# Performance work log

Measured on AMD Instinct MI355X. Metric: run time of the kernel, lower is better.

The kernel has to match this reference:

```python
import jax, jax.numpy as jnp
import numpy as np

E = 1024   # embed_dim
H = 16     # num_heads
R = 256    # rank
HD = E // H
B, S = 2, 2048


def setup_inputs() -> dict:
    key = jax.random.key(0)
    ks = jax.random.split(key, 20)
    sc = 0.02
    d = {
        'query': jax.random.normal(ks[0], (B, S, E), jnp.float32),
        'key':   jax.random.normal(ks[1], (B, S, E), jnp.float32),
        'value': jax.random.normal(ks[2], (B, S, E), jnp.float32),
    }
    names = ['q', 'k', 'v', 'o']
    i = 3
    for n in names:
        d[f'W{n}_lo'] = jax.random.normal(ks[i], (E, R), jnp.float32) * sc; i += 1
        d[f'b{n}_lo'] = jnp.zeros((R,), jnp.float32)
        d[f'W{n}_hi'] = jax.random.normal(ks[i], (R, E), jnp.float32) * sc; i += 1
        d[f'b{n}_hi'] = jnp.zeros((E,), jnp.float32)
    return d


def _lowrank(x, W_lo, b_lo, W_hi, b_hi):
    # Linear(E->R) then Linear(R->E)
    return (x @ W_lo + b_lo) @ W_hi + b_hi


def reference(query, key, value,
              Wq_lo, bq_lo, Wq_hi, bq_hi,
              Wk_lo, bk_lo, Wk_hi, bk_hi,
              Wv_lo, bv_lo, Wv_hi, bv_hi,
              Wo_lo, bo_lo, Wo_hi, bo_hi):
    b, s, _ = query.shape
    q = _lowrank(query, Wq_lo, bq_lo, Wq_hi, bq_hi)
    k = _lowrank(key,   Wk_lo, bk_lo, Wk_hi, bk_hi)
    v = _lowrank(value, Wv_lo, bv_lo, Wv_hi, bv_hi)
    # (B, S, E) -> (B, H, S, HD)
    q = q.reshape(b, s, H, HD).transpose(0, 2, 1, 3)
    k = k.reshape(b, s, H, HD).transpose(0, 2, 1, 3)
    v = v.reshape(b, s, H, HD).transpose(0, 2, 1, 3)
    scores = jnp.einsum('bhqd,bhkd->bhqk', q, k) / jnp.sqrt(jnp.float32(HD))
    attn = jax.nn.softmax(scores, axis=-1)  # dropout p=0.0 -> identity
    out = jnp.einsum('bhqk,bhkd->bhqd', attn, v)
    out = out.transpose(0, 2, 1, 3).reshape(b, s, E)
    return _lowrank(out, Wo_lo, bo_lo, Wo_hi, bo_hi)
```

## Files before the change

### kernel.cpp

```cpp
#include <hip/hip_runtime.h>

namespace {

constexpr int kE  = 1024;
constexpr int kH  = 16;
constexpr int kR  = 256;
constexpr int kHD = 64;
constexpr int kB  = 2;
constexpr int kS  = 2048;
constexpr int kM  = kB * kS;

typedef float  floatx4 __attribute__((ext_vector_type(4)));
typedef short  short8  __attribute__((ext_vector_type(8)));
typedef short  short4  __attribute__((ext_vector_type(4)));
typedef unsigned int uint2v __attribute__((ext_vector_type(2)));

__device__ inline short f2bf(float f) {
  union { float f; unsigned u; } x{f};
  unsigned r = x.u + 0x7FFF + ((x.u >> 16) & 1);
  return (short)(r >> 16);
}

__device__ inline unsigned cvt_pk_bf16(float a, float b) {
#if defined(__HIP_DEVICE_COMPILE__)
  unsigned r;
  asm("v_cvt_pk_bf16_f32 %0, %1, %2" : "=v"(r) : "v"(a), "v"(b));
  return r;
#else
  return (unsigned)(unsigned short)f2bf(a) | ((unsigned)(unsigned short)f2bf(b) << 16);
#endif
}

__device__ inline short4 pack2(unsigned a, unsigned b) {
  union { uint2v u; short4 s; } x;
  x.u[0] = a; x.u[1] = b;
  return x.s;
}

__device__ inline float fexp2(float x) {
#if defined(__HIP_DEVICE_COMPILE__) && __has_builtin(__builtin_amdgcn_exp2f)
  return __builtin_amdgcn_exp2f(x);
#else
  return exp2f(x);
#endif
}

__device__ inline void async_copy16(const void* g, void* l) {
  __builtin_amdgcn_global_load_lds(
      (const __attribute__((address_space(1))) unsigned int*)g,
      (__attribute__((address_space(3))) unsigned int*)l,
      16, 0, 0);
}

#if defined(__HIP_DEVICE_COMPILE__)
  #if __has_builtin(__builtin_amdgcn_mfma_f32_16x16x16bf16_1k)
    #define MFMA16(a, b, c) __builtin_amdgcn_mfma_f32_16x16x16bf16_1k(a, b, c, 0, 0, 0)
  #elif __has_builtin(__builtin_amdgcn_mfma_f32_16x16x16_bf16)
    #define MFMA16(a, b, c) __builtin_amdgcn_mfma_f32_16x16x16_bf16(a, b, c, 0, 0, 0)
  #else
    #error "no 16x16x16 bf16 MFMA builtin on device"
  #endif
#else
  #define MFMA16(a, b, c) (c)
#endif

struct PrepArgs { const float* src[8]; short* dst[8]; };

__global__ __launch_bounds__(256) void prep_weights(PrepArgs pa) {
  const int id = blockIdx.y;
  const bool lo = (id & 1) == 0;
  const int K = lo ? 1024 : 256;
  const int N = lo ? 256 : 1024;
  const int tiles_k = K >> 6;
  const int k0 = (blockIdx.x % tiles_k) * 64;
  const int n0 = (blockIdx.x / tiles_k) * 64;
  const float* src = pa.src[id];
  short* dst = pa.dst[id];

  __shared__ float tile[64][68];
  const int t  = threadIdx.x;
  const int c4 = (t & 15) * 4;
  const int r  = t >> 4;

#pragma unroll
  for (int i = 0; i < 4; ++i) {
    const int rk = r + i * 16;
    *(float4*)&tile[rk][c4] = *(const float4*)&src[(size_t)(k0 + rk) * N + n0 + c4];
  }
  __syncthreads();
#pragma unroll
  for (int i = 0; i < 4; ++i) {
    const int rn = r + i * 16;
    short4 o = { f2bf(tile[c4 + 0][rn]), f2bf(tile[c4 + 1][rn]),
                 f2bf(tile[c4 + 2][rn]), f2bf(tile[c4 + 3][rn]) };
    *(short4*)&dst[(size_t)(n0 + rn) * K + k0 + c4] = o;
  }
}

__global__ __launch_bounds__(256) void convert_in(
    const float* q, const float* k, const float* v,
    short* xq, short* xk, short* xv)
{
  const float* srcs[3] = {q, k, v};
  short* dsts[3] = {xq, xk, xv};
  const float* s = srcs[blockIdx.y];
  short* d = dsts[blockIdx.y];
  const size_t i = ((size_t)blockIdx.x * 256 + threadIdx.x) * 8;
  float4 a = *(const float4*)(s + i);
  float4 b = *(const float4*)(s + i + 4);
  short8 o = { f2bf(a.x), f2bf(a.y), f2bf(a.z), f2bf(a.w),
               f2bf(b.x), f2bf(b.y), f2bf(b.z), f2bf(b.w) };
  *(short8*)(d + i) = o;
}

struct GemmArgs {
  const short* A[3]; const short* Bt[3]; const float* bias[3];
  void* C[3]; float scale[3];
};

template <int N, int K, int BM, int BN, int MODE>
__global__ __launch_bounds__(256) void gemm_bf16(GemmArgs args) {
  constexpr int TILES_N = N / BN;
  constexpr int WTM = BM / 2, WTN = BN / 2;
  constexpr int FI = WTM / 16, FJ = WTN / 16;
  constexpr int AROUNDS = (BM * 64) / 4096;
  constexpr int BROUNDS = (BN * 64) / 4096;

  const int z = blockIdx.y;
  const int row0 = (blockIdx.x / TILES_N) * BM;
  const int col0 = (blockIdx.x % TILES_N) * BN;
  const short* A  = args.A[z];
  const short* Bt = args.Bt[z];
  const float* bias = args.bias[z];
  const float scale = args.scale[z];

  __shared__ short As[BM * 32];
  __shared__ short Bs[BN * 32];

  const int t    = threadIdx.x;
  const int wave = t >> 6;
  const int lane = t & 63;
  const int lq   = lane & 15;
  const int quad = lane >> 4;
  const int wm0  = (wave >> 1) * WTM;
  const int wn0  = (wave & 1) * WTN;

  const int srow = t >> 2;
  const int scol = (t & 3) * 8;

  floatx4 acc[FI][FJ] = {};

  for (int kk = 0; kk < K; kk += 32) {
#pragma unroll
    for (int r = 0; r < AROUNDS; ++r)
      async_copy16(A + (size_t)(row0 + r * 64 + srow) * K + kk + scol,
                   (char*)As + r * 4096 + wave * 1024);
#pragma unroll
    for (int r = 0; r < BROUNDS; ++r)
      async_copy16(Bt + (size_t)(col0 + r * 64 + srow) * K + kk + scol,
                   (char*)Bs + r * 4096 + wave * 1024);
    __syncthreads();

    short8 af[FI], bf[FJ];
#pragma unroll
    for (int i = 0; i < FI; ++i)
      af[i] = *(const short8*)((const char*)As + ((wm0 + i * 16 + lq) * 64 + quad * 16));
#pragma unroll
    for (int j = 0; j < FJ; ++j)
      bf[j] = *(const short8*)((const char*)Bs + ((wn0 + j * 16 + lq) * 64 + quad * 16));
#pragma unroll
    for (int i = 0; i < FI; ++i)
#pragma unroll
      for (int j = 0; j < FJ; ++j)
        acc[i][j] = __builtin_amdgcn_mfma_f32_16x16x32_bf16(af[i], bf[j], acc[i][j], 0, 0, 0);
    __syncthreads();
  }

#pragma unroll
  for (int i = 0; i < FI; ++i) {
    const int rbase = row0 + wm0 + i * 16 + quad * 4;
#pragma unroll
    for (int j = 0; j < FJ; ++j) {
      const int col = col0 + wn0 + j * 16 + lq;
      const float bj = bias[col];
      if (MODE == 2) {
        float* C = (float*)args.C[z];
#pragma unroll
        for (int r = 0; r < 4; ++r)
          C[(size_t)(rbase + r) * N + col] = (acc[i][j][r] + bj) * scale;
      } else if (MODE == 1) {
        short* C = (short*)args.C[z];
        const int h = col >> 6, d = col & 63;
        const int b = rbase >> 11, s = rbase & 2047;
        if (z == 2) {
          short4 o = { f2bf(acc[i][j][0] + bj), f2bf(acc[i][j][1] + bj),
                       f2bf(acc[i][j][2] + bj), f2bf(acc[i][j][3] + bj) };
          *(short4*)&C[((size_t)((b * 16 + h) * 64 + d)) * 2048 + s] = o;
        } else {
#pragma unroll
          for (int r = 0; r < 4; ++r)
            C[((size_t)((b * 16 + h) * 2048 + s + r)) * 64 + d] =
                f2bf((acc[i][j][r] + bj) * scale);
        }
      } else {
        short* C = (short*)args.C[z];
#pragma unroll
        for (int r = 0; r < 4; ++r)
          C[(size_t)(rbase + r) * N + col] = f2bf((acc[i][j][r] + bj) * scale);
      }
    }
  }
}

__global__ __launch_bounds__(256) void attn_mfma(
    const short* __restrict__ Qp, const short* __restrict__ Kp,
    const short* __restrict__ Vtp, short* __restrict__ O)
{
  __shared__ short Ks[64][72];
  __shared__ short Vs[64][72];

  const int t    = threadIdx.x;
  const int wave = t >> 6;
  const int lane = t & 63;
  const int lq   = lane & 15;
  const int quad = lane >> 4;

  const int q0 = blockIdx.x * 128;
  const int bh = blockIdx.y;
  const int b  = bh >> 4;
  const int h  = bh & 15;

  short8 qf0[2], qf1[2];
#pragma unroll
  for (int qt = 0; qt < 2; ++qt) {
    const short* qrow = Qp + ((size_t)bh * kS + q0 + wave * 32 + qt * 16 + lq) * 64;
    qf0[qt] = *(const short8*)(qrow + quad * 8);
    qf1[qt] = *(const short8*)(qrow + 32 + quad * 8);
  }

  const short* Kbase = Kp  + (size_t)bh * kS * 64;
  const short* Vbase = Vtp + (size_t)bh * 64 * kS;

  const int srow = wave * 16 + (lane >> 3);
  const int scol = (lane & 7) * 8;

  floatx4 Oacc[4][2] = {};
  float m[2] = {-1e30f, -1e30f};
  float l[2] = {0.f, 0.f};

  short8 gk0 = *(const short8*)(Kbase + (size_t)(srow) * 64 + scol);
  short8 gk1 = *(const short8*)(Kbase + (size_t)(srow + 8) * 64 + scol);
  short8 gv0 = *(const short8*)(Vbase + (size_t)srow * kS + scol);
  short8 gv1 = *(const short8*)(Vbase + (size_t)(srow + 8) * kS + scol);

  for (int kc = 0; kc < kS; kc += 64) {
    __syncthreads();
    *(short8*)&Ks[srow][scol]     = gk0;
    *(short8*)&Ks[srow + 8][scol] = gk1;
    *(short8*)&Vs[srow][scol]     = gv0;
    *(short8*)&Vs[srow + 8][scol] = gv1;
    __syncthreads();

    if (kc + 64 < kS) {
      gk0 = *(const short8*)(Kbase + (size_t)(kc + 64 + srow) * 64 + scol);
      gk1 = *(const short8*)(Kbase + (size_t)(kc + 64 + srow + 8) * 64 + scol);
      gv0 = *(const short8*)(Vbase + (size_t)srow * kS + kc + 64 + scol);
      gv1 = *(const short8*)(Vbase + (size_t)(srow + 8) * kS + kc + 64 + scol);
    }

    floatx4 Sc[4][2];
#pragma unroll
    for (int tt = 0; tt < 4; ++tt) {
      short8 a0 = *(const short8*)&Ks[tt * 16 + lq][quad * 8];
      short8 a1 = *(const short8*)&Ks[tt * 16 + lq][32 + quad * 8];
#pragma unroll
      for (int qt = 0; qt < 2; ++qt) {
        floatx4 c = {};
        c = __builtin_amdgcn_mfma_f32_16x16x32_bf16(a0, qf0[qt], c, 0, 0, 0);
        c = __builtin_amdgcn_mfma_f32_16x16x32_bf16(a1, qf1[qt], c, 0, 0, 0);
        Sc[tt][qt] = c;
      }
    }

    short4 pf[4][2];
#pragma unroll
    for (int qt = 0; qt < 2; ++qt) {
      float x0 = fmaxf(fmaxf(Sc[0][qt][0], Sc[0][qt][1]), fmaxf(Sc[0][qt][2], Sc[0][qt][3]));
      float x1 = fmaxf(fmaxf(Sc[1][qt][0], Sc[1][qt][1]), fmaxf(Sc[1][qt][2], Sc[1][qt][3]));
      float x2 = fmaxf(fmaxf(Sc[2][qt][0], Sc[2][qt][1]), fmaxf(Sc[2][qt][2], Sc[2][qt][3]));
      float x3 = fmaxf(fmaxf(Sc[3][qt][0], Sc[3][qt][1]), fmaxf(Sc[3][qt][2], Sc[3][qt][3]));
      float plane = fmaxf(fmaxf(x0, x1), fmaxf(x2, x3));

      if (!__all(plane <= m[qt] + 10.f)) {
        float mc = fmaxf(plane, __shfl_xor(plane, 16, 64));
        mc = fmaxf(mc, __shfl_xor(mc, 32, 64));
        const float mn = fmaxf(m[qt], mc);
        const float a = fexp2(m[qt] - mn);
        m[qt] = mn;
        l[qt] *= a;
#pragma unroll
        for (int dt = 0; dt < 4; ++dt) Oacc[dt][qt] *= a;
      }

      float ls = 0.f;
#pragma unroll
      for (int tt = 0; tt < 4; ++tt) {
        float p0 = fexp2(Sc[tt][qt][0] - m[qt]);
        float p1 = fexp2(Sc[tt][qt][1] - m[qt]);
        float p2 = fexp2(Sc[tt][qt][2] - m[qt]);
        float p3 = fexp2(Sc[tt][qt][3] - m[qt]);
        ls += (p0 + p1) + (p2 + p3);
        pf[tt][qt] = pack2(cvt_pk_bf16(p0, p1), cvt_pk_bf16(p2, p3));
      }
      l[qt] += ls;
    }

#pragma unroll
    for (int dt = 0; dt < 4; ++dt) {
#pragma unroll
      for (int tt = 0; tt < 4; ++tt) {
        short4 vf = *(const short4*)&Vs[dt * 16 + lq][tt * 16 + quad * 4];
#pragma unroll
        for (int qt = 0; qt < 2; ++qt)
          Oacc[dt][qt] = MFMA16(vf, pf[tt][qt], Oacc[dt][qt]);
      }
    }
  }

#pragma unroll
  for (int qt = 0; qt < 2; ++qt) {
    float lv = l[qt];
    lv += __shfl_xor(lv, 16, 64);
    lv += __shfl_xor(lv, 32, 64);
    const float inv = 1.f / lv;

    short* orow = O + ((size_t)(b * kS + q0 + wave * 32 + qt * 16 + lq)) * kE + h * kHD;
#pragma unroll
    for (int dt = 0; dt < 4; ++dt) {
      short4 o = pack2(cvt_pk_bf16(Oacc[dt][qt][0] * inv, Oacc[dt][qt][1] * inv),
                       cvt_pk_bf16(Oacc[dt][qt][2] * inv, Oacc[dt][qt][3] * inv));
      *(short4*)&orow[dt * 16 + quad * 4] = o;
    }
  }
}

}

extern "C" void kernel_launch(void* const* d_in, const int* in_sizes, int n_in,
                              void* d_out, int out_size, void* d_ws, size_t ws_size,
                              hipStream_t stream) {
  short* ws = (short*)d_ws;
  short* Xq  = ws;
  short* Xk  = Xq  + (size_t)kM * kE;
  short* Xv  = Xk  + (size_t)kM * kE;
  short* Tq  = Xv  + (size_t)kM * kE;
  short* Tk  = Tq  + (size_t)kM * kR;
  short* Tv  = Tk  + (size_t)kM * kR;
  short* Qh  = Tv  + (size_t)kM * kR;
  short* Kh  = Qh  + (size_t)kM * kE;
  short* Vth = Kh  + (size_t)kM * kE;
  short* Ab  = Vth + (size_t)kM * kE;
  short* To  = Ab  + (size_t)kM * kE;
  short* Wt  = To  + (size_t)kM * kR;

  short* WtArr[8];
  for (int i = 0; i < 8; ++i) WtArr[i] = Wt + (size_t)i * (kE * kR);

  PrepArgs pa;
  const int widx[8] = {3, 5, 7, 9, 11, 13, 15, 17};
  for (int i = 0; i < 8; ++i) { pa.src[i] = (const float*)d_in[widx[i]]; pa.dst[i] = WtArr[i]; }
  prep_weights<<<dim3(64, 8), dim3(256), 0, stream>>>(pa);

  convert_in<<<dim3((kM * kE) / (256 * 8), 3), dim3(256), 0, stream>>>(
      (const float*)d_in[0], (const float*)d_in[1], (const float*)d_in[2], Xq, Xk, Xv);

  {
    GemmArgs ga;
    ga.A[0] = Xq; ga.A[1] = Xk; ga.A[2] = Xv;
    ga.Bt[0] = WtArr[0]; ga.Bt[1] = WtArr[2]; ga.Bt[2] = WtArr[4];
    ga.bias[0] = (const float*)d_in[4]; ga.bias[1] = (const float*)d_in[8]; ga.bias[2] = (const float*)d_in[12];
    ga.C[0] = Tq; ga.C[1] = Tk; ga.C[2] = Tv;
    ga.scale[0] = ga.scale[1] = ga.scale[2] = 1.f;
    gemm_bf16<kR, kE, 64, 64, 0><<<dim3((kM / 64) * (kR / 64), 3), dim3(256), 0, stream>>>(ga);
  }

  {
    GemmArgs ga;
    ga.A[0] = Tq; ga.A[1] = Tk; ga.A[2] = Tv;
    ga.Bt[0] = WtArr[1]; ga.Bt[1] = WtArr[3]; ga.Bt[2] = WtArr[5];
    ga.bias[0] = (const float*)d_in[6]; ga.bias[1] = (const float*)d_in[10]; ga.bias[2] = (const float*)d_in[14];
    ga.C[0] = Qh; ga.C[1] = Kh; ga.C[2] = Vth;
    ga.scale[0] = 0.125f * 1.44269504088896340736f;
    ga.scale[1] = 1.f; ga.scale[2] = 1.f;
    gemm_bf16<kE, kR, 128, 128, 1><<<dim3((kM / 128) * (kE / 128), 3), dim3(256), 0, stream>>>(ga);
  }

  attn_mfma<<<dim3(kS / 128, kB * kH), dim3(256), 0, stream>>>(Qh, Kh, Vth, Ab);

  {
    GemmArgs ga;
    ga.A[0] = Ab; ga.Bt[0] = WtArr[6];
    ga.bias[0] = (const float*)d_in[16];
    ga.C[0] = To; ga.scale[0] = 1.f;
    gemm_bf16<kR, kE, 64, 64, 0><<<dim3((kM / 64) * (kR / 64), 1), dim3(256), 0, stream>>>(ga);
  }
  {
    GemmArgs ga;
    ga.A[0] = To; ga.Bt[0] = WtArr[7];
    ga.bias[0] = (const float*)d_in[18];
    ga.C[0] = d_out; ga.scale[0] = 1.f;
    gemm_bf16<kE, kR, 128, 128, 2><<<dim3((kM / 128) * (kE / 128), 1), dim3(256), 0, stream>>>(ga);
  }
}
```

Measured before the change: 250.8 us.

## Fuse fp32-to-bf16 input conversion into the low-rank projection GEMM

Removes the standalone convert_in kernel and adds a GEMM that loads fp32 activations directly, converting them to bf16 while reading from shared memory before the MFMA. This eliminates the intermediate bf16 copy of query/key/value and one kernel launch. In exchange, each A tile is re-read in fp32 by every column-tile block, and the new kernel uses a simple register-prefetch loop with two barriers per K step.

New measurement: 256.1 us. 2.1% more time.

```diff
diff --git a/kernel.cpp b/kernel.cpp
--- a/kernel.cpp
+++ b/kernel.cpp
@@ -34,6 +34,12 @@
 __device__ inline short4 pack2(unsigned a, unsigned b) {
   union { uint2v u; short4 s; } x;
   x.u[0] = a; x.u[1] = b;
+  return x.s;
+}
+
+__device__ inline short8 pack4(unsigned a, unsigned b, unsigned c, unsigned d) {
+  union { unsigned u[4]; short8 s; } x;
+  x.u[0] = a; x.u[1] = b; x.u[2] = c; x.u[3] = d;
   return x.s;
 }
 
@@ -97,22 +103,6 @@
   }
 }
 
-__global__ __launch_bounds__(256) void convert_in(
-    const float* q, const float* k, const float* v,
-    short* xq, short* xk, short* xv)
-{
-  const float* srcs[3] = {q, k, v};
-  short* dsts[3] = {xq, xk, xv};
-  const float* s = srcs[blockIdx.y];
-  short* d = dsts[blockIdx.y];
-  const size_t i = ((size_t)blockIdx.x * 256 + threadIdx.x) * 8;
-  float4 a = *(const float4*)(s + i);
-  float4 b = *(const float4*)(s + i + 4);
-  short8 o = { f2bf(a.x), f2bf(a.y), f2bf(a.z), f2bf(a.w),
-               f2bf(b.x), f2bf(b.y), f2bf(b.z), f2bf(b.w) };
-  *(short8*)(d + i) = o;
-}
-
 struct GemmArgs {
   const short* A[3]; const short* Bt[3]; const float* bias[3];
   void* C[3]; float scale[3];
@@ -208,6 +198,92 @@
         for (int r = 0; r < 4; ++r)
           C[(size_t)(rbase + r) * N + col] = f2bf((acc[i][j][r] + bj) * scale);
       }
+    }
+  }
+}
+
+struct GemmLoArgs {
+  const float* A[3]; const short* Bt[3]; const float* bias[3]; short* C[3];
+};
+
+__global__ __launch_bounds__(256) void gemm_lo_f32a(GemmLoArgs args) {
+  constexpr int N = kR, K = kE, BM = 64, BN = 64;
+  constexpr int TILES_N = N / BN;
+  constexpr int WTM = BM / 2, WTN = BN / 2;
+  constexpr int FI = WTM / 16, FJ = WTN / 16;
+
+  const int z = blockIdx.y;
+  const int row0 = (blockIdx.x / TILES_N) * BM;
+  const int col0 = (blockIdx.x % TILES_N) * BN;
+  const float* A  = args.A[z];
+  const short* Bt = args.Bt[z];
+  const float* bias = args.bias[z];
+  short* C = args.C[z];
+
+  __shared__ float As32[64][36];
+  __shared__ short Bs[BN * 32];
+
+  const int t    = threadIdx.x;
+  const int wave = t >> 6;
+  const int lane = t & 63;
+  const int lq   = lane & 15;
+  const int quad = lane >> 4;
+  const int wm0  = (wave >> 1) * WTM;
+  const int wn0  = (wave & 1) * WTN;
+
+  const int arow  = t >> 2;
+  const int acolf = (t & 3) * 8;
+  const int srow = t >> 2;
+  const int scol = (t & 3) * 8;
+
+  floatx4 acc[FI][FJ] = {};
+
+  const float* arow_p = A + (size_t)(row0 + arow) * K + acolf;
+  float4 ga0 = *(const float4*)(arow_p);
+  float4 ga1 = *(const float4*)(arow_p + 4);
+
+  for (int kk = 0; kk < K; kk += 32) {
+    __syncthreads();
+    *(float4*)&As32[arow][acolf]     = ga0;
+    *(float4*)&As32[arow][acolf + 4] = ga1;
+    async_copy16(Bt + (size_t)(col0 + srow) * K + kk + scol,
+                 (char*)Bs + wave * 1024);
+    __syncthreads();
+
+    if (kk + 32 < K) {
+      ga0 = *(const float4*)(arow_p + kk + 32);
+      ga1 = *(const float4*)(arow_p + kk + 36);
+    }
+
+    short8 af[FI], bf[FJ];
+#pragma unroll
+    for (int i = 0; i < FI; ++i) {
+      const int r = wm0 + i * 16 + lq;
+      float4 f0 = *(const float4*)&As32[r][quad * 8];
+      float4 f1 = *(const float4*)&As32[r][quad * 8 + 4];
+      af[i] = pack4(cvt_pk_bf16(f0.x, f0.y), cvt_pk_bf16(f0.z, f0.w),
+                    cvt_pk_bf16(f1.x, f1.y), cvt_pk_bf16(f1.z, f1.w));
+    }
+#pragma unroll
+    for (int j = 0; j < FJ; ++j)
+      bf[j] = *(const short8*)((const char*)Bs + ((wn0 + j * 16 + lq) * 64 + quad * 16));
+#pragma unroll
+    for (int i = 0; i < FI; ++i)
+#pragma unroll
+      for (int j = 0; j < FJ; ++j)
+        acc[i][j] = __builtin_amdgcn_mfma_f32_16x16x32_bf16(af[i], bf[j], acc[i][j], 0, 0, 0);
+  }
+
+#pragma unroll
+  for (int i = 0; i < FI; ++i) {
+    const int rbase = row0 + wm0 + i * 16 + quad * 4;
+#pragma unroll
+    for (int j = 0; j < FJ; ++j) {
+      const int col = col0 + wn0 + j * 16 + lq;
+      const float bj = bias[col];
+#pragma unroll
+      for (int r = 0; r < 4; ++r)
+        C[(size_t)(rbase + r) * N + col] = f2bf(acc[i][j][r] + bj);
     }
   }
 }
@@ -362,6 +438,7 @@
   short* Ab  = Vth + (size_t)kM * kE;
   short* To  = Ab  + (size_t)kM * kE;
   short* Wt  = To  + (size_t)kM * kR;
+  (void)Xk; (void)Xv;
 
   short* WtArr[8];
   for (int i = 0; i < 8; ++i) WtArr[i] = Wt + (size_t)i * (kE * kR);
@@ -371,17 +448,13 @@
   for (int i = 0; i < 8; ++i) { pa.src[i] = (const float*)d_in[widx[i]]; pa.dst[i] = WtArr[i]; }
   prep_weights<<<dim3(64, 8), dim3(256), 0, stream>>>(pa);
 
-  convert_in<<<dim3((kM * kE) / (256 * 8), 3), dim3(256), 0, stream>>>(
-      (const float*)d_in[0], (const float*)d_in[1], (const float*)d_in[2], Xq, Xk, Xv);
-
   {
-    GemmArgs ga;
-    ga.A[0] = Xq; ga.A[1] = Xk; ga.A[2] = Xv;
+    GemmLoArgs ga;
+    ga.A[0] = (const float*)d_in[0]; ga.A[1] = (const float*)d_in[1]; ga.A[2] = (const float*)d_in[2];
     ga.Bt[0] = WtArr[0]; ga.Bt[1] = WtArr[2]; ga.Bt[2] = WtArr[4];
     ga.bias[0] = (const float*)d_in[4]; ga.bias[1] = (const float*)d_in[8]; ga.bias[2] = (const float*)d_in[12];
     ga.C[0] = Tq; ga.C[1] = Tk; ga.C[2] = Tv;
-    ga.scale[0] = ga.scale[1] = ga.scale[2] = 1.f;
-    gemm_bf16<kR, kE, 64, 64, 0><<<dim3((kM / 64) * (kR / 64), 3), dim3(256), 0, stream>>>(ga);
+    gemm_lo_f32a<<<dim3((kM / 64) * (kR / 64), 3), dim3(256), 0, stream>>>(ga);
   }
 
   {
```

## Fold low-rank projection pairs into dense E×E weights and swizzle GEMM tiles across XCDs

Applied to the files above, without the earlier changes.

Each call now multiplies W_hi^T by W_lo^T in a small GEMM to form a dense 1024×1024 bf16 weight per projection. It also folds b_lo through W_hi into a combined bias. The Q/K/V and output projections then become one dense GEMM each instead of two chained GEMMs, which removes the rank-256 intermediate buffers and two launches. The cost is about double the projection FLOPs, plus an extra weight-combine GEMM and different bf16 rounding. GEMM block indices are also remapped so consecutive tiles spread across the 8 XCDs.

After: 281.4 us. 12.2% more time.

```diff
diff --git a/kernel.cpp b/kernel.cpp
--- a/kernel.cpp
+++ b/kernel.cpp
@@ -50,6 +50,10 @@
       (const __attribute__((address_space(1))) unsigned int*)g,
       (__attribute__((address_space(3))) unsigned int*)l,
       16, 0, 0);
+}
+
+__device__ inline int xcd_swz256(int bid) {
+  return ((bid & 7) << 5) | (bid >> 3);
 }
 
 #if defined(__HIP_DEVICE_COMPILE__)
@@ -64,14 +68,12 @@
   #define MFMA16(a, b, c) (c)
 #endif
 
-struct PrepArgs { const float* src[8]; short* dst[8]; };
+struct PrepArgs { const float* src[4]; short* dst[4]; };
 
 __global__ __launch_bounds__(256) void prep_weights(PrepArgs pa) {
   const int id = blockIdx.y;
-  const bool lo = (id & 1) == 0;
-  const int K = lo ? 1024 : 256;
-  const int N = lo ? 256 : 1024;
-  const int tiles_k = K >> 6;
+  constexpr int K = 256, N = 1024;
+  constexpr int tiles_k = K >> 6;
   const int k0 = (blockIdx.x % tiles_k) * 64;
   const int n0 = (blockIdx.x / tiles_k) * 64;
   const float* src = pa.src[id];
@@ -94,6 +96,36 @@
     short4 o = { f2bf(tile[c4 + 0][rn]), f2bf(tile[c4 + 1][rn]),
                  f2bf(tile[c4 + 2][rn]), f2bf(tile[c4 + 3][rn]) };
     *(short4*)&dst[(size_t)(n0 + rn) * K + k0 + c4] = o;
+  }
+}
+
+struct AuxArgs {
+  const float* wlo[4]; const float* blo[4];
+  const float* whi[4]; const float* bhi[4];
+  short* wloF; float* cb; float* zb;
+};
+
+__global__ __launch_bounds__(256) void aux_prep(AuxArgs a) {
+  const int y = blockIdx.y, bx = blockIdx.x, t = threadIdx.x;
+  if (y < 4) {
+    const float* s = a.wlo[y];
+    short* d = a.wloF + (size_t)y * (kE * kR);
+    const size_t i = ((size_t)bx * 256 + t) * 8;
+    float4 p = *(const float4*)(s + i);
+    float4 q = *(const float4*)(s + i + 4);
+    short8 o = { f2bf(p.x), f2bf(p.y), f2bf(p.z), f2bf(p.w),
+                 f2bf(q.x), f2bf(q.y), f2bf(q.z), f2bf(q.w) };
+    *(short8*)(d + i) = o;
+  } else if (bx < 16) {
+    const int i = bx >> 2;
+    const int n = ((bx & 3) << 8) + t;
+    const float* blo = a.blo[i];
+    const float* whi = a.whi[i];
+    float s = a.bhi[i][n];
+    for (int r = 0; r < 256; ++r) s += blo[r] * whi[r * 1024 + n];
+    a.cb[i * 1024 + n] = s;
+  } else if (bx == 16) {
+    for (int j = t; j < 1024; j += 256) a.zb[j] = 0.f;
   }
 }
 
@@ -114,21 +146,24 @@
 }
 
 struct GemmArgs {
-  const short* A[3]; const short* Bt[3]; const float* bias[3];
-  void* C[3]; float scale[3];
+  const short* A[4]; const short* Bt[4]; const float* bias[4];
+  void* C[4]; float scale[4];
 };
 
-template <int N, int K, int BM, int BN, int MODE>
+template <int M, int N, int K, int BM, int BN, int MODE>
 __global__ __launch_bounds__(256) void gemm_bf16(GemmArgs args) {
   constexpr int TILES_N = N / BN;
   constexpr int WTM = BM / 2, WTN = BN / 2;
   constexpr int FI = WTM / 16, FJ = WTN / 16;
   constexpr int AROUNDS = (BM * 64) / 4096;
   constexpr int BROUNDS = (BN * 64) / 4096;
+  static_assert((M / BM) * (N / BN) == 256, "swizzle assumes nwg=256");
+  static_assert(MODE != 1 || M == kM, "MODE1 decode assumes M=4096");
 
   const int z = blockIdx.y;
-  const int row0 = (blockIdx.x / TILES_N) * BM;
-  const int col0 = (blockIdx.x % TILES_N) * BN;
+  const int swz = xcd_swz256(blockIdx.x);
+  const int row0 = (swz / TILES_N) * BM;
+  const int col0 = (swz % TILES_N) * BN;
   const short* A  = args.A[z];
   const short* Bt = args.Bt[z];
   const float* bias = args.bias[z];
@@ -349,66 +384,84 @@
 extern "C" void kernel_launch(void* const* d_in, const int* in_sizes, int n_in,
                               void* d_out, int out_size, void* d_ws, size_t ws_size,
                               hipStream_t stream) {
-  short* ws = (short*)d_ws;
-  short* Xq  = ws;
-  short* Xk  = Xq  + (size_t)kM * kE;
-  short* Xv  = Xk  + (size_t)kM * kE;
-  short* Tq  = Xv  + (size_t)kM * kE;
-  short* Tk  = Tq  + (size_t)kM * kR;
-  short* Tv  = Tk  + (size_t)kM * kR;
-  short* Qh  = Tv  + (size_t)kM * kR;
-  short* Kh  = Qh  + (size_t)kM * kE;
-  short* Vth = Kh  + (size_t)kM * kE;
-  short* Ab  = Vth + (size_t)kM * kE;
-  short* To  = Ab  + (size_t)kM * kE;
-  short* Wt  = To  + (size_t)kM * kR;
-
-  short* WtArr[8];
-  for (int i = 0; i < 8; ++i) WtArr[i] = Wt + (size_t)i * (kE * kR);
-
-  PrepArgs pa;
-  const int widx[8] = {3, 5, 7, 9, 11, 13, 15, 17};
-  for (int i = 0; i < 8; ++i) { pa.src[i] = (const float*)d_in[widx[i]]; pa.dst[i] = WtArr[i]; }
-  prep_weights<<<dim3(64, 8), dim3(256), 0, stream>>>(pa);
+  constexpr size_t SZ = (size_t)kM * kE;
+  short* ws   = (short*)d_ws;
+  short* Xq   = ws;
+  short* Xk   = Xq  + SZ;
+  short* Xv   = Xk  + SZ;
+  short* Qh   = Xv  + SZ;
+  short* Kh   = Qh  + SZ;
+  short* Vth  = Kh  + SZ;
+  short* Ab   = Vth + SZ;
+  short* WloF = Ab;
+  short* WhiT = Ab  + SZ;
+  short* Wct  = WhiT + 4 * (size_t)(kE * kR);
+  float* cb   = (float*)(Wct + 4 * (size_t)(kE * kE));
+  float* zb   = cb + 4 * 1024;
+
+  {
+    PrepArgs pa;
+    const int whidx[4] = {5, 9, 13, 17};
+    for (int i = 0; i < 4; ++i) {
+      pa.src[i] = (const float*)d_in[whidx[i]];
+      pa.dst[i] = WhiT + (size_t)i * (kE * kR);
+    }
+    prep_weights<<<dim3(64, 4), dim3(256), 0, stream>>>(pa);
+  }
+
+  {
+    AuxArgs aa;
+    const int wlidx[4] = {3, 7, 11, 15};
+    const int blidx[4] = {4, 8, 12, 16};
+    const int whidx[4] = {5, 9, 13, 17};
+    const int bhidx[4] = {6, 10, 14, 18};
+    for (int i = 0; i < 4; ++i) {
+      aa.wlo[i] = (const float*)d_in[wlidx[i]];
+      aa.blo[i] = (const float*)d_in[blidx[i]];
+      aa.whi[i] = (const float*)d_in[whidx[i]];
+      aa.bhi[i] = (const float*)d_in[bhidx[i]];
+    }
+    aa.wloF = WloF; aa.cb = cb; aa.zb = zb;
+    aux_prep<<<dim3(128, 5), dim3(256), 0, stream>>>(aa);
+  }
 
   convert_in<<<dim3((kM * kE) / (256 * 8), 3), dim3(256), 0, stream>>>(
       (const float*)d_in[0], (const float*)d_in[1], (const float*)d_in[2], Xq, Xk, Xv);
+
+  {
+    GemmArgs ga;
+    for (int i = 0; i < 4; ++i) {
+      ga.A[i]    = WhiT + (size_t)i * (kE * kR);
+      ga.Bt[i]   = WloF + (size_t)i * (kE * kR);
+      ga.bias[i] = zb;
+      ga.C[i]    = Wct + (size_t)i * (kE * kE);
+      ga.scale[i] = 1.f;
+    }
+    gemm_bf16<kE, kE, kR, 64, 64, 0><<<dim3(256, 4), dim3(256), 0, stream>>>(ga);
+  }
 
   {
     GemmArgs ga;
     ga.A[0] = Xq; ga.A[1] = Xk; ga.A[2] = Xv;
-    ga.Bt[0] = WtArr[0]; ga.Bt[1] = WtArr[2]; ga.Bt[2] = WtArr[4];
-    ga.bias[0] = (const float*)d_in[4]; ga.bias[1] = (const float*)d_in[8]; ga.bias[2] = (const float*)d_in[12];
-    ga.C[0] = Tq; ga.C[1] = Tk; ga.C[2] = Tv;
-    ga.scale[0] = ga.scale[1] = ga.scale[2] = 1.f;
-    gemm_bf16<kR, kE, 64, 64, 0><<<dim3((kM / 64) * (kR / 64), 3), dim3(256), 0, stream>>>(ga);
-  }
-
-  {
-    GemmArgs ga;
-    ga.A[0] = Tq; ga.A[1] = Tk; ga.A[2] = Tv;
-    ga.Bt[0] = WtArr[1]; ga.Bt[1] = WtArr[3]; ga.Bt[2] = WtArr[5];
-    ga.bias[0] = (const float*)d_in[6]; ga.bias[1] = (const float*)d_in[10]; ga.bias[2] = (const float*)d_in[14];
+    for (int i = 0; i < 3; ++i) {
+      ga.Bt[i]   = Wct + (size_t)i * (kE * kE);
+      ga.bias[i] = cb + i * 1024;
+    }
     ga.C[0] = Qh; ga.C[1] = Kh; ga.C[2] = Vth;
     ga.scale[0] = 0.125f * 1.44269504088896340736f;
     ga.scale[1] = 1.f; ga.scale[2] = 1.f;
-    gemm_bf16<kE, kR, 128, 128, 1><<<dim3((kM / 128) * (kE / 128), 3), dim3(256), 0, stream>>>(ga);
+    gemm_bf16<kM, kE, kE, 128, 128, 1><<<dim3(256, 3), dim3(256), 0, stream>>>(ga);
   }
 
   attn_mfma<<<dim3(kS / 128, kB * kH), dim3(256), 0, stream>>>(Qh, Kh, Vth, Ab);
 
   {
     GemmArgs ga;
-    ga.A[0] = Ab; ga.Bt[0] = WtArr[6];
-    ga.bias[0] = (const float*)d_in[16];
-    ga.C[0] = To; ga.scale[0] = 1.f;
-    gemm_bf16<kR, kE, 64, 64, 0><<<dim3((kM / 64) * (kR / 64), 1), dim3(256), 0, stream>>>(ga);
-  }
-  {
-    GemmArgs ga;
-    ga.A[0] = To; ga.Bt[0] = WtArr[7];
-    ga.bias[0] = (const float*)d_in[18];
-    ga.C[0] = d_out; ga.scale[0] = 1.f;
-    gemm_bf16<kE, kR, 128, 128, 2><<<dim3((kM / 128) * (kE / 128), 1), dim3(256), 0, stream>>>(ga);
-  }
-}
+    ga.A[0]    = Ab;
+    ga.Bt[0]   = Wct + (size_t)3 * (kE * kE);
+    ga.bias[0] = cb + 3 * 1024;
+    ga.C[0]    = d_out;
+    ga.scale[0] = 1.f;
+    gemm_bf16<kM, kE, kE, 128, 128, 2><<<dim3(256, 1), dim3(256), 0, stream>>>(ga);
+  }
+}
```
